# Kernel optimization log

Measured on AMD Instinct MI355X. Metric: run time of the kernel, lower is better.

Reference implementation:

```python
import jax, jax.numpy as jnp
import numpy as np

N = 300000        # active voxels
C = 64            # channels (in_dim == out_dim)
K = 27            # 3x3x3 kernel offsets
EPS = 1e-5        # BatchNorm eps
GX, GY, GZ = 256, 256, 32  # voxel grid


def _build_neighbors():
    """Submanifold rulebook: for each active voxel, index of the active voxel at
    each of the 27 offsets, or -1 if that neighbor voxel is inactive."""
    rng = np.random.default_rng(0)
    lin = np.sort(rng.choice(GX * GY * GZ, size=N, replace=False))
    x, y, z = lin // (GY * GZ), (lin // GZ) % GY, lin % GZ
    nbr = np.full((N, K), -1, dtype=np.int32)
    k = 0
    for dx in (-1, 0, 1):
        for dy in (-1, 0, 1):
            for dz in (-1, 0, 1):
                nx, ny, nz = x + dx, y + dy, z + dz
                inb = (nx >= 0) & (nx < GX) & (ny >= 0) & (ny < GY) & (nz >= 0) & (nz < GZ)
                nl = (nx * GY + ny) * GZ + nz
                pos = np.searchsorted(lin, nl)
                posc = np.clip(pos, 0, N - 1)
                found = inb & (lin[posc] == nl)
                nbr[:, k] = np.where(found, posc, -1)
                k += 1
    return jnp.asarray(nbr)


def setup_inputs() -> dict:
    key = jax.random.key(0)
    k0, k1, k2 = jax.random.split(key, 3)
    return {
        "feats": jax.random.normal(k0, (N, C), dtype=jnp.float32),
        "W1": jax.random.normal(k1, (K, C, C), dtype=jnp.float32) * 0.05,
        "gamma1": jnp.ones((C,), jnp.float32),
        "beta1": jnp.zeros((C,), jnp.float32),
        "W2": jax.random.normal(k2, (K, C, C), dtype=jnp.float32) * 0.05,
        "gamma2": jnp.ones((C,), jnp.float32),
        "beta2": jnp.zeros((C,), jnp.float32),
        "neighbor_idx": _build_neighbors(),
    }


def _subm_conv(feats, W, nbr):
    # gather -> matmul -> accumulate, one pass per kernel offset (fixed K=27)
    mask = nbr >= 0
    idx = jnp.where(mask, nbr, 0)
    out = jnp.zeros((feats.shape[0], W.shape[-1]), feats.dtype)
    for k in range(K):
        g = feats[idx[:, k]] * mask[:, k:k + 1].astype(feats.dtype)  # [N, C]
        out = out + g @ W[k]
    return out


def _bn_relu(x, gamma, beta):
    # BatchNorm1d training-mode forward: biased batch stats over active voxels
    mu = jnp.mean(x, axis=0)
    var = jnp.var(x, axis=0)
    return jax.nn.relu((x - mu) * jax.lax.rsqrt(var + EPS) * gamma + beta)


def reference(feats, W1, gamma1, beta1, W2, gamma2, beta2, neighbor_idx):
    x_net = _bn_relu(_subm_conv(feats, W1, neighbor_idx), gamma1, beta1)
    res = _bn_relu(_subm_conv(x_net, W2, neighbor_idx), gamma2, beta2)
    return x_net + res
```

## Files before the change

### kernel.cpp

```cpp
#include <hip/hip_runtime.h>
#include <cstdint>
#include <cstddef>

typedef unsigned short u16;
typedef __bf16 bf16x8 __attribute__((ext_vector_type(8)));
typedef float f32x4 __attribute__((ext_vector_type(4)));

#define KOFF 27
#define EPSBN 1e-5f

__device__ inline u16 f2bf(float f) {
  unsigned int u = __float_as_uint(f);
  unsigned int r = (u + 0x7FFFu + ((u >> 16) & 1u)) >> 16;
  return (u16)r;
}
__device__ inline float bf2f(u16 h) {
  return __uint_as_float(((unsigned int)h) << 16);
}

__global__ void k_prep(const float* __restrict__ feats, const float* __restrict__ W1,
                       const float* __restrict__ W2, const int* __restrict__ nbr,
                       u16* __restrict__ featsb, u16* __restrict__ w1p,
                       u16* __restrict__ w2p, int* __restrict__ nbrT,
                       float* __restrict__ stats, int N, int gN, int gW, int n4) {
  __shared__ int L[64 * KOFF];
  const int t = threadIdx.x;
  const int bid = blockIdx.x;

  if (bid < gN) {
    const int v0 = bid * 64;
    const int nv = min(64, N - v0);
    const int cnt = nv * KOFF;
    for (int i = t; i < cnt; i += 256) L[i] = nbr[(size_t)v0 * KOFF + i];
    __syncthreads();
    for (int i = t; i < KOFF * 64; i += 256) {
      int k = i >> 6, j = i & 63;
      if (j < nv) nbrT[(size_t)k * N + v0 + j] = L[j * KOFF + k];
    }
    return;
  }
  if (bid < gN + 2 * gW) {
    const int wi = bid - gN;
    const bool second = wi >= gW;
    const float* W = second ? W2 : W1;
    u16* Wp = second ? w2p : w1p;
    const int tid = (second ? wi - gW : wi) * 256 + t;
    if (tid >= KOFF * 4096) return;
    const int k = tid >> 12;
    const int rem = tid & 4095;
    const int slot = rem >> 3;
    const int e = rem & 7;
    const int ks = slot >> 8;
    const int ct = (slot >> 6) & 3;
    const int lane = slot & 63;
    const int j = ks * 32 + ((lane >> 4) << 3) + e;
    const int c = ct * 16 + (lane & 15);
    Wp[tid] = f2bf(W[(k * 64 + j) * 64 + c]);
    return;
  }
  const int idx = bid - gN - 2 * gW;
  if (idx == 0) stats[t] = 0.f;
  const int i = idx * 256 + t;
  if (i >= n4) return;
  const float4 v = reinterpret_cast<const float4*>(feats)[i];
  ushort4 o;
  o.x = f2bf(v.x); o.y = f2bf(v.y); o.z = f2bf(v.z); o.w = f2bf(v.w);
  reinterpret_cast<ushort4*>(featsb)[i] = o;
}

__launch_bounds__(256, 3)
__global__ void k_conv(const u16* __restrict__ F, const u16* __restrict__ Wp,
                       const int* __restrict__ nbrT, u16* __restrict__ rawout,
                       float* __restrict__ stats, int N) {
  const int t = threadIdx.x;
  const int w = t >> 6;
  const int lane = t & 63;
  const int vbase = blockIdx.x * 256 + (w << 6) + (lane & 15);
  const int ch = (lane >> 4) << 3;

  f32x4 acc[4][4];
#pragma unroll
  for (int m = 0; m < 4; ++m)
#pragma unroll
    for (int c = 0; c < 4; ++c) acc[m][c] = (f32x4){0.f, 0.f, 0.f, 0.f};

  int nid[4];
#pragma unroll
  for (int m = 0; m < 4; ++m) {
    const int v = vbase + (m << 4);
    nid[m] = (v < N) ? nbrT[v] : -1;
  }

  const u16* bp = Wp + ((size_t)lane << 3);

#pragma unroll 3
  for (int k = 0; k < KOFF; ++k) {
    bf16x8 bfr[2][4];
#pragma unroll
    for (int ks = 0; ks < 2; ++ks)
#pragma unroll
      for (int c = 0; c < 4; ++c)
        bfr[ks][c] = *reinterpret_cast<const bf16x8*>(bp + ((size_t)k << 12) + (ks << 11) + (c << 9));

    bf16x8 a0[4], a1[4];
#pragma unroll
    for (int m = 0; m < 4; ++m) {
      a0[m] = (bf16x8){};
      a1[m] = (bf16x8){};
      const int id = nid[m];
      if (id >= 0) {
        const u16* fr = F + ((size_t)id << 6) + ch;
        a0[m] = *reinterpret_cast<const bf16x8*>(fr);
        a1[m] = *reinterpret_cast<const bf16x8*>(fr + 32);
      }
    }

    if (k + 1 < KOFF) {
      const int* nk = nbrT + (size_t)(k + 1) * N;
#pragma unroll
      for (int m = 0; m < 4; ++m) {
        const int v = vbase + (m << 4);
        nid[m] = (v < N) ? nk[v] : -1;
      }
    }

#pragma unroll
    for (int m = 0; m < 4; ++m)
#pragma unroll
      for (int c = 0; c < 4; ++c)
        acc[m][c] = __builtin_amdgcn_mfma_f32_16x16x32_bf16(a0[m], bfr[0][c], acc[m][c], 0, 0, 0);
#pragma unroll
    for (int m = 0; m < 4; ++m)
#pragma unroll
      for (int c = 0; c < 4; ++c)
        acc[m][c] = __builtin_amdgcn_mfma_f32_16x16x32_bf16(a1[m], bfr[1][c], acc[m][c], 0, 0, 0);
  }

  const int row0 = blockIdx.x * 256 + (w << 6) + ((lane >> 4) << 2);
  const bool evenlane = (lane & 1) == 0;
#pragma unroll
  for (int m = 0; m < 4; ++m) {
#pragma unroll
    for (int e = 0; e < 4; ++e) {
      const int v = row0 + (m << 4) + e;
#pragma unroll
      for (int c = 0; c < 4; ++c) {
        const unsigned myb = (unsigned)f2bf(acc[m][c][e]);
        const unsigned ob = (unsigned)__shfl_xor((int)myb, 1, 64);
        if (evenlane && v < N) {
          const int col = (c << 4) + (lane & 15);
          *reinterpret_cast<unsigned*>(rawout + ((size_t)v << 6) + col) = myb | (ob << 16);
        }
      }
    }
  }

  __shared__ float sred[4][128];
#pragma unroll
  for (int c = 0; c < 4; ++c) {
    float s = 0.f, q = 0.f;
#pragma unroll
    for (int m = 0; m < 4; ++m)
#pragma unroll
      for (int e = 0; e < 4; ++e) {
        const float x = acc[m][c][e];
        s += x;
        q += x * x;
      }
    s += __shfl_xor(s, 16, 64);
    s += __shfl_xor(s, 32, 64);
    q += __shfl_xor(q, 16, 64);
    q += __shfl_xor(q, 32, 64);
    if (lane < 16) {
      sred[w][(c << 4) + lane] = s;
      sred[w][64 + (c << 4) + lane] = q;
    }
  }
  __syncthreads();
  if (t < 128) {
    const float tot = sred[0][t] + sred[1][t] + sred[2][t] + sred[3][t];
    atomicAdd(&stats[t], tot);
  }
}


__global__ void k_apply1(const u16* __restrict__ raw, const float* __restrict__ stats,
                         const float* __restrict__ gamma, const float* __restrict__ beta,
                         u16* __restrict__ xb, int n8, float invN) {
  int i = blockIdx.x * 256 + threadIdx.x;
  if (i >= n8) return;
  const int c0 = (i & 7) << 3;
  float sc[8], bi[8];
#pragma unroll
  for (int j = 0; j < 8; ++j) {
    const int c = c0 + j;
    const float mu = stats[c] * invN;
    const float var = stats[64 + c] * invN - mu * mu;
    sc[j] = gamma[c] * rsqrtf(var + EPSBN);
    bi[j] = beta[c] - mu * sc[j];
  }
  const uint4 rv = reinterpret_cast<const uint4*>(raw)[i];
  const unsigned vals[4] = {rv.x, rv.y, rv.z, rv.w};
  unsigned ov[4];
#pragma unroll
  for (int j = 0; j < 4; ++j) {
    const float lo = bf2f((u16)(vals[j] & 0xffff));
    const float hi = bf2f((u16)(vals[j] >> 16));
    const float y0 = fmaxf(0.f, lo * sc[2 * j] + bi[2 * j]);
    const float y1 = fmaxf(0.f, hi * sc[2 * j + 1] + bi[2 * j + 1]);
    ov[j] = (unsigned)f2bf(y0) | ((unsigned)f2bf(y1) << 16);
  }
  reinterpret_cast<uint4*>(xb)[i] = make_uint4(ov[0], ov[1], ov[2], ov[3]);
}

__global__ void k_apply2(const u16* __restrict__ raw, const float* __restrict__ stats,
                         const float* __restrict__ gamma, const float* __restrict__ beta,
                         const u16* __restrict__ xb, float* __restrict__ out, int n8,
                         float invN) {
  int i = blockIdx.x * 256 + threadIdx.x;
  if (i >= n8) return;
  const int c0 = (i & 7) << 3;
  float sc[8], bi[8];
#pragma unroll
  for (int j = 0; j < 8; ++j) {
    const int c = c0 + j;
    const float mu = stats[c] * invN;
    const float var = stats[64 + c] * invN - mu * mu;
    sc[j] = gamma[c] * rsqrtf(var + EPSBN);
    bi[j] = beta[c] - mu * sc[j];
  }
  const uint4 rv = reinterpret_cast<const uint4*>(raw)[i];
  const uint4 xv = reinterpret_cast<const uint4*>(xb)[i];
  const unsigned rvals[4] = {rv.x, rv.y, rv.z, rv.w};
  const unsigned xvals[4] = {xv.x, xv.y, xv.z, xv.w};
  float o[8];
#pragma unroll
  for (int j = 0; j < 4; ++j) {
    const float rlo = bf2f((u16)(rvals[j] & 0xffff));
    const float rhi = bf2f((u16)(rvals[j] >> 16));
    o[2 * j] = bf2f((u16)(xvals[j] & 0xffff)) + fmaxf(0.f, rlo * sc[2 * j] + bi[2 * j]);
    o[2 * j + 1] = bf2f((u16)(xvals[j] >> 16)) + fmaxf(0.f, rhi * sc[2 * j + 1] + bi[2 * j + 1]);
  }
  reinterpret_cast<float4*>(out)[2 * i] = make_float4(o[0], o[1], o[2], o[3]);
  reinterpret_cast<float4*>(out)[2 * i + 1] = make_float4(o[4], o[5], o[6], o[7]);
}


extern "C" void kernel_launch(void* const* d_in, const int* in_sizes, int n_in,
                              void* d_out, int out_size, void* d_ws, size_t ws_size,
                              hipStream_t stream) {
  const float* feats = (const float*)d_in[0];
  const float* W1 = (const float*)d_in[1];
  const float* g1 = (const float*)d_in[2];
  const float* b1 = (const float*)d_in[3];
  const float* W2 = (const float*)d_in[4];
  const float* g2 = (const float*)d_in[5];
  const float* b2 = (const float*)d_in[6];
  const int* nbr = (const int*)d_in[7];
  const int N = in_sizes[0] / 64;

  char* ws = (char*)d_ws;
  size_t off = 0;
  auto alloc = [&](size_t bytes) {
    void* p = ws + off;
    off = (off + bytes + 255) & ~(size_t)255;
    return p;
  };
  u16* featsb = (u16*)alloc((size_t)N * 64 * 2);
  u16* xnetb = (u16*)alloc((size_t)N * 64 * 2);
  u16* w1p = (u16*)alloc((size_t)KOFF * 4096 * 2);
  u16* w2p = (u16*)alloc((size_t)KOFF * 4096 * 2);
  float* stats = (float*)alloc(256 * 4);
  int* nbrT = (int*)alloc((size_t)KOFF * N * 4);

  u16* raw1 = (u16*)d_out;
  u16* raw2 = featsb;
  float* outf = (float*)d_out;

  const int n4 = N * 16;
  const int n8 = N * 8;
  const float invN = 1.0f / (float)N;
  const int gN = (N + 63) / 64;
  const int gPrep = (n4 + 255) / 256;
  const int gApply = (n8 + 255) / 256;
  const int gW = (KOFF * 4096 + 255) / 256;
  const int gConv = (N + 255) / 256;

  k_prep<<<gN + 2 * gW + gPrep, 256, 0, stream>>>(feats, W1, W2, nbr, featsb, w1p, w2p,
                                                  nbrT, stats, N, gN, gW, n4);

  k_conv<<<gConv, 256, 0, stream>>>(featsb, w1p, nbrT, raw1, stats, N);
  k_apply1<<<gApply, 256, 0, stream>>>(raw1, stats, g1, b1, xnetb, n8, invN);

  k_conv<<<gConv, 256, 0, stream>>>(xnetb, w2p, nbrT, raw2, stats + 128, N);
  k_apply2<<<gApply, 256, 0, stream>>>(raw2, stats + 128, g2, b2, xnetb, outf, n8, invN);
}
```

Before: 248.2 us.

## Software-pipeline neighbor feature gathers across kernel offsets in sparse conv

Restructures the conv loop so the feature gathers for the next offset are issued between the two halves of the current offset's MFMA work. The neighbor index list is prefetched two offsets ahead, using an extra sentinel row of -1 appended to the transposed rulebook. MFMA sections are wrapped in s_setprio to favour the matrix issue stream. The aim is to hide gather latency behind matrix math, at the cost of higher register pressure and the loss of the unroll-3 loop.

Result: slower. 294.9 us (+18.8%).

```diff
diff --git a/kernel.cpp b/kernel.cpp
--- a/kernel.cpp
+++ b/kernel.cpp
@@ -37,6 +37,7 @@
       int k = i >> 6, j = i & 63;
       if (j < nv) nbrT[(size_t)k * N + v0 + j] = L[j * KOFF + k];
     }
+    if (t < nv) nbrT[(size_t)KOFF * N + v0 + t] = -1;
     return;
   }
   if (bid < gN + 2 * gW) {
@@ -84,46 +85,91 @@
 #pragma unroll
     for (int c = 0; c < 4; ++c) acc[m][c] = (f32x4){0.f, 0.f, 0.f, 0.f};
 
+  bool vok[4];
   int nid[4];
 #pragma unroll
   for (int m = 0; m < 4; ++m) {
     const int v = vbase + (m << 4);
-    nid[m] = (v < N) ? nbrT[v] : -1;
+    vok[m] = v < N;
+    nid[m] = vok[m] ? nbrT[v] : -1;
+  }
+
+  bf16x8 a0[4], a1[4];
+#pragma unroll
+  for (int m = 0; m < 4; ++m) {
+    a0[m] = (bf16x8){};
+    a1[m] = (bf16x8){};
+    if (nid[m] >= 0) {
+      const u16* fr = F + ((size_t)(unsigned)nid[m] << 6) + ch;
+      a0[m] = *reinterpret_cast<const bf16x8*>(fr);
+      a1[m] = *reinterpret_cast<const bf16x8*>(fr + 32);
+    }
+  }
+  {
+    const int* nk = nbrT + (size_t)N;
+#pragma unroll
+    for (int m = 0; m < 4; ++m) nid[m] = vok[m] ? nk[vbase + (m << 4)] : -1;
   }
 
   const u16* bp = Wp + ((size_t)lane << 3);
 
-#pragma unroll 3
-  for (int k = 0; k < KOFF; ++k) {
+  for (int k = 0; k < 26; ++k) {
     bf16x8 bfr[2][4];
+    {
+      const u16* bk = bp + ((size_t)k << 12);
+#pragma unroll
+      for (int ks = 0; ks < 2; ++ks)
+#pragma unroll
+        for (int c = 0; c < 4; ++c)
+          bfr[ks][c] = *reinterpret_cast<const bf16x8*>(bk + (ks << 11) + (c << 9));
+    }
+    const int ids[4] = {nid[0], nid[1], nid[2], nid[3]};
+    __builtin_amdgcn_s_setprio(1);
+#pragma unroll
+    for (int m = 0; m < 4; ++m)
+#pragma unroll
+      for (int c = 0; c < 4; ++c)
+        acc[m][c] = __builtin_amdgcn_mfma_f32_16x16x32_bf16(a0[m], bfr[0][c], acc[m][c], 0, 0, 0);
+    __builtin_amdgcn_s_setprio(0);
+    const u16* srcs[4];
+#pragma unroll
+    for (int m = 0; m < 4; ++m) {
+      bf16x8 v = (bf16x8){};
+      if (ids[m] >= 0) {
+        srcs[m] = F + ((size_t)(unsigned)ids[m] << 6) + ch;
+        v = *reinterpret_cast<const bf16x8*>(srcs[m]);
+      }
+      a0[m] = v;
+    }
+    __builtin_amdgcn_s_setprio(1);
+#pragma unroll
+    for (int m = 0; m < 4; ++m)
+#pragma unroll
+      for (int c = 0; c < 4; ++c)
+        acc[m][c] = __builtin_amdgcn_mfma_f32_16x16x32_bf16(a1[m], bfr[1][c], acc[m][c], 0, 0, 0);
+    __builtin_amdgcn_s_setprio(0);
+#pragma unroll
+    for (int m = 0; m < 4; ++m) {
+      bf16x8 v = (bf16x8){};
+      if (ids[m] >= 0) v = *reinterpret_cast<const bf16x8*>(srcs[m] + 32);
+      a1[m] = v;
+    }
+    {
+      const int* nk = nbrT + (size_t)(k + 2) * N;
+#pragma unroll
+      for (int m = 0; m < 4; ++m) nid[m] = vok[m] ? nk[vbase + (m << 4)] : -1;
+    }
+  }
+
+  {
+    bf16x8 bfr[2][4];
+    const u16* bk = bp + ((size_t)26 << 12);
 #pragma unroll
     for (int ks = 0; ks < 2; ++ks)
 #pragma unroll
       for (int c = 0; c < 4; ++c)
-        bfr[ks][c] = *reinterpret_cast<const bf16x8*>(bp + ((size_t)k << 12) + (ks << 11) + (c << 9));
-
-    bf16x8 a0[4], a1[4];
-#pragma unroll
-    for (int m = 0; m < 4; ++m) {
-      a0[m] = (bf16x8){};
-      a1[m] = (bf16x8){};
-      const int id = nid[m];
-      if (id >= 0) {
-        const u16* fr = F + ((size_t)id << 6) + ch;
-        a0[m] = *reinterpret_cast<const bf16x8*>(fr);
-        a1[m] = *reinterpret_cast<const bf16x8*>(fr + 32);
-      }
-    }
-
-    if (k + 1 < KOFF) {
-      const int* nk = nbrT + (size_t)(k + 1) * N;
-#pragma unroll
-      for (int m = 0; m < 4; ++m) {
-        const int v = vbase + (m << 4);
-        nid[m] = (v < N) ? nk[v] : -1;
-      }
-    }
-
+        bfr[ks][c] = *reinterpret_cast<const bf16x8*>(bk + (ks << 11) + (c << 9));
+    __builtin_amdgcn_s_setprio(1);
 #pragma unroll
     for (int m = 0; m < 4; ++m)
 #pragma unroll
@@ -134,6 +180,7 @@
 #pragma unroll
       for (int c = 0; c < 4; ++c)
         acc[m][c] = __builtin_amdgcn_mfma_f32_16x16x32_bf16(a1[m], bfr[1][c], acc[m][c], 0, 0, 0);
+    __builtin_amdgcn_s_setprio(0);
   }
 
   const int row0 = blockIdx.x * 256 + (w << 6) + ((lane >> 4) << 2);
@@ -271,7 +318,7 @@
   u16* w1p = (u16*)alloc((size_t)KOFF * 4096 * 2);
   u16* w2p = (u16*)alloc((size_t)KOFF * 4096 * 2);
   float* stats = (float*)alloc(256 * 4);
-  int* nbrT = (int*)alloc((size_t)KOFF * N * 4);
+  int* nbrT = (int*)alloc((size_t)(KOFF + 1) * N * 4);
 
   u16* raw1 = (u16*)d_out;
   u16* raw2 = featsb;
```
